# Optimization experiments

Measured on AMD Instinct MI355X. Metric: run time of the kernel, lower is better.

Reference implementation:

```python
import jax, jax.numpy as jnp
import numpy as np

WINDOW_SIZE = 11

def _gauss_window(ws):
    x = np.arange(ws, dtype=np.float32)
    g = np.exp(-0.5 * (x - (ws - 1) / 2.0) ** 2 / 0.5 ** 2)
    g = g / g.sum()
    w = np.outer(g, g)
    return jnp.asarray(w[None, None], dtype=jnp.float32)  # [1,1,ws,ws]

_SOBEL_X = jnp.asarray(np.array([[-1, 0, 1], [-2, 0, 2], [-1, 0, 1]], np.float32)[None, None])
_SOBEL_Y = jnp.asarray(np.array([[1, 2, 1], [0, 0, 0], [-1, -2, -1]], np.float32)[None, None])

def _conv2d(x, k, pad):
    # x: [B,1,H,W], k: [1,1,kh,kw], 'same'-style explicit padding
    return jax.lax.conv_general_dilated(
        x, k, window_strides=(1, 1), padding=[(pad, pad), (pad, pad)],
        dimension_numbers=("NCHW", "OIHW", "NCHW"))

def _sobel(x):
    return jnp.abs(_conv2d(x, _SOBEL_X, 1)) + jnp.abs(_conv2d(x, _SOBEL_Y, 1))

def setup_inputs() -> dict:
    key = jax.random.key(0)
    kA, kB, kF, kS = jax.random.split(key, 4)
    shape = (32, 1, 512, 512)
    return {
        "image_A": jax.random.uniform(kA, shape, dtype=jnp.float32),
        "image_B": jax.random.uniform(kB, shape, dtype=jnp.float32),
        "image_fused": jax.random.uniform(kF, shape, dtype=jnp.float32),
        "fuse_scheme": jax.random.randint(kS, (32,), 0, 2, dtype=jnp.int64),
    }

def reference(image_A, image_B, image_fused, fuse_scheme):
    ws = WINDOW_SIZE
    pad = ws // 2
    window = _gauss_window(ws)
    scheme = fuse_scheme.reshape(-1, 1, 1, 1)

    # masked construction of the pseudo-reference image_AB
    avg_AB = (image_A + image_B) * 0.5
    max_AB = jnp.maximum(image_A, image_B)
    image_AB = jnp.where(scheme == 0, avg_AB,
                         jnp.where(scheme == 1, max_AB, jnp.zeros_like(image_fused)))
    l_loss = jnp.mean(jnp.abs(image_AB - image_fused))

    # SSIM-style local statistics
    mu_A = _conv2d(image_A, window, pad)
    mu_B = _conv2d(image_B, window, pad)
    mu_f = _conv2d(image_fused, window, pad)
    sigma_A_sq = _conv2d(image_A ** 2, window, pad) - mu_A ** 2
    sigma_B_sq = _conv2d(image_B ** 2, window, pad) - mu_B ** 2
    sigma_f_sq = _conv2d(image_fused ** 2, window, pad) - mu_f ** 2
    sigma_Af = _conv2d(image_A * image_fused, window, pad) - mu_A * mu_f
    sigma_Bf = _conv2d(image_B * image_fused, window, pad) - mu_B * mu_f

    C = 0.03 ** 2
    cs1 = (2 * sigma_Af + C) / (sigma_A_sq + sigma_f_sq + C)
    cs2 = (2 * sigma_Bf + C) / (sigma_B_sq + sigma_f_sq + C)
    cs_map = 0.5 * cs1 + 0.5 * cs2
    cs_loss = 1.0 - (cs_map.mean() + 1.0) / 2.0

    grad_loss = jnp.mean(jnp.abs(_sobel(image_fused) -
                                 jnp.maximum(_sobel(image_A), _sobel(image_B))))
    return l_loss + 0.0 * cs_loss + grad_loss
```

## Files before the change

### kernel.cpp

```cpp
#include <hip/hip_runtime.h>

#define BATCH 32
#define H 512
#define W 512
#define N_TOT (BATCH * H * W)
#define ROWS_TOTAL (BATCH * H)
#define NBLOCKS (ROWS_TOTAL / 4)
#define WS_FLOATS NBLOCKS


template <bool USE_PARTIALS>
__global__ __launch_bounds__(256)
void fusion_loss_kernel(const float* __restrict__ A,
                        const float* __restrict__ B,
                        const float* __restrict__ F,
                        const int* __restrict__ scheme_arr,
                        float* __restrict__ sink)
{
    __shared__ float red[4];

    const int t    = threadIdx.x;
    const int lane = t & 63;
    const int ty   = t >> 6;

    const int bid = blockIdx.x;
    const int lb  = (bid & 7) * (NBLOCKS / 8) + (bid >> 3);

    const int gy  = (lb << 2) | ty;
    const int b   = gy >> 9;
    const int y   = gy & (H - 1);
    const int scheme = scheme_arr[b];
    const int off = gy * W + (lane << 3);

    const float* pA = A + off;
    const float* pB = B + off;
    const float* pF = F + off;
    const bool vm = (y > 0);
    const bool vp = (y < H - 1);

    const float4 z4 = make_float4(0.f, 0.f, 0.f, 0.f);

#define LD2(d0_, d1_, p_) do {                                              \
    d0_ = *reinterpret_cast<const float4*>(p_);                             \
    d1_ = *reinterpret_cast<const float4*>((p_) + 4);                       \
} while (0)
#define LDROW(d0_, d1_, p_, v_) do {                                        \
    if (v_) LD2(d0_, d1_, p_); else { d0_ = z4; d1_ = z4; }                 \
} while (0)

#define SOBH(JB_, T0,T1,T2,T3,T4,T5, C0,C1,C2,C3,C4,C5,                     \
             Q0,Q1,Q2,Q3,Q4,Q5, ...) do {                                   \
    const float s_[6] = {(T0) + 2.f*(C0) + (Q0), (T1) + 2.f*(C1) + (Q1),    \
                         (T2) + 2.f*(C2) + (Q2), (T3) + 2.f*(C3) + (Q3),    \
                         (T4) + 2.f*(C4) + (Q4), (T5) + 2.f*(C5) + (Q5)};   \
    const float d_[6] = {(T0) - (Q0), (T1) - (Q1), (T2) - (Q2),             \
                         (T3) - (Q3), (T4) - (Q4), (T5) - (Q5)};            \
    _Pragma("unroll")                                                       \
    for (int j = 0; j < 4; ++j) {                                           \
        const int jj = (JB_) + j; (void)jj;                                 \
        const float gx  = s_[j + 2] - s_[j];                                \
        const float gyv = d_[j] + 2.f * d_[j + 1] + d_[j + 2];              \
        const float sob = fabsf(gx) + fabsf(gyv);                           \
        __VA_ARGS__;                                                        \
    }                                                                       \
} while (0)

#define SOBEL(...) do {                                                     \
    float lt_ = __shfl_up(m1.w, 1, 64),  rt_ = __shfl_down(m0.x, 1, 64);    \
    float lc_ = __shfl_up(c1.w, 1, 64),  rc_ = __shfl_down(c0.x, 1, 64);    \
    float lq_ = __shfl_up(p1.w, 1, 64),  rq_ = __shfl_down(p0.x, 1, 64);    \
    if (lane == 0)  { lt_ = 0.f; lc_ = 0.f; lq_ = 0.f; }                    \
    if (lane == 63) { rt_ = 0.f; rc_ = 0.f; rq_ = 0.f; }                    \
    SOBH(0, lt_, m0.x, m0.y, m0.z, m0.w, m1.x,                              \
            lc_, c0.x, c0.y, c0.z, c0.w, c1.x,                              \
            lq_, p0.x, p0.y, p0.z, p0.w, p1.x, __VA_ARGS__);                \
    SOBH(4, m0.w, m1.x, m1.y, m1.z, m1.w, rt_,                              \
            c0.w, c1.x, c1.y, c1.z, c1.w, rc_,                              \
            p0.w, p1.x, p1.y, p1.z, p1.w, rq_, __VA_ARGS__);                \
} while (0)

    float4 m0, m1, c0, c1, p0, p1;
    float4 bc0, bc1, fc0, fc1;
    float  sobM[8];
    float  acc = 0.f;

    LDROW(m0, m1, pA - W, vm);
    LD2(c0, c1, pA);
    LDROW(p0, p1, pA + W, vp);
    LD2(bc0, bc1, pB);
    LD2(fc0, fc1, pF);

    {
        const float av[8] = {c0.x, c0.y, c0.z, c0.w, c1.x, c1.y, c1.z, c1.w};
        const float bv[8] = {bc0.x, bc0.y, bc0.z, bc0.w,
                             bc1.x, bc1.y, bc1.z, bc1.w};
        const float fv[8] = {fc0.x, fc0.y, fc0.z, fc0.w,
                             fc1.x, fc1.y, fc1.z, fc1.w};
#pragma unroll
        for (int j = 0; j < 8; ++j) {
            const float ab = (scheme == 0) ? 0.5f * (av[j] + bv[j])
                           : (scheme == 1) ? fmaxf(av[j], bv[j])
                           : 0.f;
            acc += fabsf(ab - fv[j]);
        }
    }

    SOBEL(sobM[jj] = sob);
    __builtin_amdgcn_sched_barrier(0);

    LDROW(m0, m1, pB - W, vm);
    c0 = bc0; c1 = bc1;
    LDROW(p0, p1, pB + W, vp);
    SOBEL(sobM[jj] = fmaxf(sobM[jj], sob));
    __builtin_amdgcn_sched_barrier(0);

    LDROW(m0, m1, pF - W, vm);
    c0 = fc0; c1 = fc1;
    LDROW(p0, p1, pF + W, vp);
    SOBEL(acc += fabsf(sob - sobM[jj]));

#undef LD2
#undef LDROW
#undef SOBH
#undef SOBEL

#pragma unroll
    for (int offp = 32; offp > 0; offp >>= 1)
        acc += __shfl_down(acc, offp, 64);
    if (lane == 0) red[ty] = acc;
    __syncthreads();
    if (t == 0) {
        const float s = red[0] + red[1] + red[2] + red[3];
        if (USE_PARTIALS)
            sink[bid] = s;
        else
            atomicAdd(sink, s * (1.0f / (float)N_TOT));
    }
}

__global__ __launch_bounds__(256)
void fusion_finish(const float* __restrict__ partials, float* __restrict__ out)
{
    __shared__ float red[4];
    const int t    = threadIdx.x;
    const int lane = t & 63;
    const int ty   = t >> 6;

    float s = 0.f;
#pragma unroll
    for (int k = 0; k < 4; ++k) {
        const float4 p = reinterpret_cast<const float4*>(partials)[t + 256 * k];
        s += (p.x + p.y) + (p.z + p.w);
    }
#pragma unroll
    for (int off = 32; off > 0; off >>= 1)
        s += __shfl_down(s, off, 64);
    if (lane == 0) red[ty] = s;
    __syncthreads();
    if (t == 0)
        out[0] = (red[0] + red[1] + red[2] + red[3]) * (1.0f / (float)N_TOT);
}

extern "C" void kernel_launch(void* const* d_in, const int* in_sizes, int n_in,
                              void* d_out, int out_size, void* d_ws, size_t ws_size,
                              hipStream_t stream)
{
    const float* A = (const float*)d_in[0];
    const float* B = (const float*)d_in[1];
    const float* F = (const float*)d_in[2];
    const int* scheme = (const int*)d_in[3];
    float* out = (float*)d_out;

    if (d_ws != nullptr && ws_size >= WS_FLOATS * sizeof(float)) {
        float* partials = (float*)d_ws;
        fusion_loss_kernel<true><<<dim3(NBLOCKS), dim3(256), 0, stream>>>(
            A, B, F, scheme, partials);
        fusion_finish<<<dim3(1), dim3(256), 0, stream>>>(partials, out);
    } else {
        hipMemsetAsync(out, 0, sizeof(float), stream);
        fusion_loss_kernel<false><<<dim3(NBLOCKS), dim3(256), 0, stream>>>(
            A, B, F, scheme, out);
    }
}
```

Measured before the change: 128.6 us.

## Process two output rows per wavefront to reuse vertical Sobel halo rows

Each wavefront now computes two adjacent image rows, loading four input rows per image instead of three for one row. This cuts redundant halo row loads from 3x to 2x per output row and halves the block count. The launch bounds also request 4 waves per SIMD occupancy hint. The cost is more registers per thread and fewer blocks in flight, and the scheduling barriers between phases are dropped.

Result: no change. 128.7 us (+0.1%).

```diff
diff --git a/kernel.cpp b/kernel.cpp
--- a/kernel.cpp
+++ b/kernel.cpp
@@ -4,13 +4,13 @@
 #define H 512
 #define W 512
 #define N_TOT (BATCH * H * W)
-#define ROWS_TOTAL (BATCH * H)
-#define NBLOCKS (ROWS_TOTAL / 4)
+#define PAIRS_TOTAL (BATCH * H / 2)
+#define NBLOCKS (PAIRS_TOTAL / 4)
 #define WS_FLOATS NBLOCKS
 
 
 template <bool USE_PARTIALS>
-__global__ __launch_bounds__(256)
+__global__ __launch_bounds__(256, 4)
 void fusion_loss_kernel(const float* __restrict__ A,
                         const float* __restrict__ B,
                         const float* __restrict__ F,
@@ -26,7 +26,8 @@
     const int bid = blockIdx.x;
     const int lb  = (bid & 7) * (NBLOCKS / 8) + (bid >> 3);
 
-    const int gy  = (lb << 2) | ty;
+    const int gp  = (lb << 2) | ty;
+    const int gy  = gp << 1;
     const int b   = gy >> 9;
     const int y   = gy & (H - 1);
     const int scheme = scheme_arr[b];
@@ -36,7 +37,7 @@
     const float* pB = B + off;
     const float* pF = F + off;
     const bool vm = (y > 0);
-    const bool vp = (y < H - 1);
+    const bool vq = (y < H - 2);
 
     const float4 z4 = make_float4(0.f, 0.f, 0.f, 0.f);
 
@@ -46,6 +47,13 @@
 } while (0)
 #define LDROW(d0_, d1_, p_, v_) do {                                        \
     if (v_) LD2(d0_, d1_, p_); else { d0_ = z4; d1_ = z4; }                 \
+} while (0)
+
+#define HALO(l_, r_, r0_, r1_) do {                                         \
+    l_ = __shfl_up((r1_).w, 1, 64);                                         \
+    r_ = __shfl_down((r0_).x, 1, 64);                                       \
+    if (lane == 0)  l_ = 0.f;                                               \
+    if (lane == 63) r_ = 0.f;                                               \
 } while (0)
 
 #define SOBH(JB_, T0,T1,T2,T3,T4,T5, C0,C1,C2,C3,C4,C5,                     \
@@ -65,64 +73,72 @@
     }                                                                       \
 } while (0)
 
-#define SOBEL(...) do {                                                     \
-    float lt_ = __shfl_up(m1.w, 1, 64),  rt_ = __shfl_down(m0.x, 1, 64);    \
-    float lc_ = __shfl_up(c1.w, 1, 64),  rc_ = __shfl_down(c0.x, 1, 64);    \
-    float lq_ = __shfl_up(p1.w, 1, 64),  rq_ = __shfl_down(p0.x, 1, 64);    \
-    if (lane == 0)  { lt_ = 0.f; lc_ = 0.f; lq_ = 0.f; }                    \
-    if (lane == 63) { rt_ = 0.f; rc_ = 0.f; rq_ = 0.f; }                    \
-    SOBH(0, lt_, m0.x, m0.y, m0.z, m0.w, m1.x,                              \
-            lc_, c0.x, c0.y, c0.z, c0.w, c1.x,                              \
-            lq_, p0.x, p0.y, p0.z, p0.w, p1.x, __VA_ARGS__);                \
-    SOBH(4, m0.w, m1.x, m1.y, m1.z, m1.w, rt_,                              \
-            c0.w, c1.x, c1.y, c1.z, c1.w, rc_,                              \
-            p0.w, p1.x, p1.y, p1.z, p1.w, rq_, __VA_ARGS__);                \
-} while (0)
-
-    float4 m0, m1, c0, c1, p0, p1;
-    float4 bc0, bc1, fc0, fc1;
-    float  sobM[8];
+#define SOBROW(JB_, t0,t1,lt,rt, c0_,c1_,lc,rc, q0,q1,lq,rq, ...) do {      \
+    SOBH(JB_, lt, (t0).x, (t0).y, (t0).z, (t0).w, (t1).x,                   \
+              lc, (c0_).x, (c0_).y, (c0_).z, (c0_).w, (c1_).x,              \
+              lq, (q0).x, (q0).y, (q0).z, (q0).w, (q1).x, __VA_ARGS__);     \
+    SOBH((JB_) + 4, (t0).w, (t1).x, (t1).y, (t1).z, (t1).w, rt,             \
+              (c0_).w, (c1_).x, (c1_).y, (c1_).z, (c1_).w, rc,              \
+              (q0).w, (q1).x, (q1).y, (q1).z, (q1).w, rq, __VA_ARGS__);     \
+} while (0)
+
+#define PHASE(P_, ...) do {                                                 \
+    float lm, rm, lc, rc, ld, rd, lq, rq;                                   \
+    HALO(lm, rm, m0, m1);                                                   \
+    HALO(lc, rc, c0, c1);                                                   \
+    HALO(ld, rd, d0, d1);                                                   \
+    HALO(lq, rq, q0, q1);                                                   \
+    SOBROW(0, m0, m1, lm, rm, c0, c1, lc, rc, d0, d1, ld, rd, __VA_ARGS__); \
+    SOBROW(8, c0, c1, lc, rc, d0, d1, ld, rd, q0, q1, lq, rq, __VA_ARGS__); \
+} while (0)
+
+    float4 m0, m1, c0, c1, d0, d1, q0, q1;
+    float4 aC[4], bC[4];
+    float  sobM[16];
     float  acc = 0.f;
 
     LDROW(m0, m1, pA - W, vm);
     LD2(c0, c1, pA);
-    LDROW(p0, p1, pA + W, vp);
-    LD2(bc0, bc1, pB);
-    LD2(fc0, fc1, pF);
-
+    LD2(d0, d1, pA + W);
+    LDROW(q0, q1, pA + 2 * W, vq);
+    PHASE(A, sobM[jj] = sob);
+    aC[0] = c0; aC[1] = c1; aC[2] = d0; aC[3] = d1;
+
+    LDROW(m0, m1, pB - W, vm);
+    LD2(c0, c1, pB);
+    LD2(d0, d1, pB + W);
+    LDROW(q0, q1, pB + 2 * W, vq);
+    PHASE(B, sobM[jj] = fmaxf(sobM[jj], sob));
+    bC[0] = c0; bC[1] = c1; bC[2] = d0; bC[3] = d1;
+
+    LDROW(m0, m1, pF - W, vm);
+    LD2(c0, c1, pF);
+    LD2(d0, d1, pF + W);
+    LDROW(q0, q1, pF + 2 * W, vq);
     {
-        const float av[8] = {c0.x, c0.y, c0.z, c0.w, c1.x, c1.y, c1.z, c1.w};
-        const float bv[8] = {bc0.x, bc0.y, bc0.z, bc0.w,
-                             bc1.x, bc1.y, bc1.z, bc1.w};
-        const float fv[8] = {fc0.x, fc0.y, fc0.z, fc0.w,
-                             fc1.x, fc1.y, fc1.z, fc1.w};
-#pragma unroll
-        for (int j = 0; j < 8; ++j) {
-            const float ab = (scheme == 0) ? 0.5f * (av[j] + bv[j])
-                           : (scheme == 1) ? fmaxf(av[j], bv[j])
-                           : 0.f;
-            acc += fabsf(ab - fv[j]);
+        const float4 fC[4] = {c0, c1, d0, d1};
+#pragma unroll
+        for (int k = 0; k < 4; ++k) {
+            const float av[4] = {aC[k].x, aC[k].y, aC[k].z, aC[k].w};
+            const float bv[4] = {bC[k].x, bC[k].y, bC[k].z, bC[k].w};
+            const float fv[4] = {fC[k].x, fC[k].y, fC[k].z, fC[k].w};
+#pragma unroll
+            for (int j = 0; j < 4; ++j) {
+                const float ab = (scheme == 0) ? 0.5f * (av[j] + bv[j])
+                               : (scheme == 1) ? fmaxf(av[j], bv[j])
+                               : 0.f;
+                acc += fabsf(ab - fv[j]);
+            }
         }
     }
-
-    SOBEL(sobM[jj] = sob);
-    __builtin_amdgcn_sched_barrier(0);
-
-    LDROW(m0, m1, pB - W, vm);
-    c0 = bc0; c1 = bc1;
-    LDROW(p0, p1, pB + W, vp);
-    SOBEL(sobM[jj] = fmaxf(sobM[jj], sob));
-    __builtin_amdgcn_sched_barrier(0);
-
-    LDROW(m0, m1, pF - W, vm);
-    c0 = fc0; c1 = fc1;
-    LDROW(p0, p1, pF + W, vp);
-    SOBEL(acc += fabsf(sob - sobM[jj]));
+    PHASE(F, acc += fabsf(sob - sobM[jj]));
 
 #undef LD2
 #undef LDROW
+#undef HALO
 #undef SOBH
-#undef SOBEL
+#undef SOBROW
+#undef PHASE
 
 #pragma unroll
     for (int offp = 32; offp > 0; offp >>= 1)
@@ -148,7 +164,7 @@
 
     float s = 0.f;
 #pragma unroll
-    for (int k = 0; k < 4; ++k) {
+    for (int k = 0; k < 2; ++k) {
         const float4 p = reinterpret_cast<const float4*>(partials)[t + 256 * k];
         s += (p.x + p.y) + (p.z + p.w);
     }
```
